# Optimization experiments

Hardware: AMD Instinct MI355X
Metric: run time of the kernel (lower is better)

## Reference

```python
import jax, jax.numpy as jnp
import numpy as np

B, T, D, H = 2, 2048, 1024, 16
HD = D // H
SCALE = HD ** -0.5
NEG_INF = float(np.finfo(np.float32).min)


def setup_inputs() -> dict:
    key = jax.random.key(0)
    ks = jax.random.split(key, 10)
    s = 1.0 / np.sqrt(D)
    x = jax.random.normal(ks[0], (B, T, D), dtype=jnp.float32)
    # causal mask, True = keep, shape (B,1,T,T)
    mask = jnp.broadcast_to(jnp.tril(jnp.ones((T, T), dtype=bool)), (B, 1, T, T))
    Wq = jax.random.normal(ks[1], (D, D), dtype=jnp.float32) * s
    bq = jax.random.normal(ks[2], (D,), dtype=jnp.float32) * s
    Wk = jax.random.normal(ks[3], (D, D), dtype=jnp.float32) * s
    bk = jax.random.normal(ks[4], (D,), dtype=jnp.float32) * s
    Wv = jax.random.normal(ks[5], (D, D), dtype=jnp.float32) * s
    bv = jax.random.normal(ks[6], (D,), dtype=jnp.float32) * s
    Wo = jax.random.normal(ks[7], (D, D), dtype=jnp.float32) * s
    bo = jax.random.normal(ks[8], (D,), dtype=jnp.float32) * s
    return {"x": x, "mask": mask, "Wq": Wq, "bq": bq, "Wk": Wk, "bk": bk,
            "Wv": Wv, "bv": bv, "Wo": Wo, "bo": bo}


def _split_heads(t):
    # (B,T,D) -> (B,H,T,HD)
    return t.reshape(B, T, H, HD).transpose(0, 2, 1, 3)


def masked_rowwise_softmax(scores, mask):
    # mask: bool, True = keep; fully-masked rows return zeros.
    s = scores.astype(jnp.float32)
    masked = jnp.where(mask, s, NEG_INF)
    row_max = jnp.max(masked, axis=-1, keepdims=True)
    exps = jnp.exp(masked - row_max) * mask.astype(jnp.float32)
    denom = jnp.maximum(jnp.sum(exps, axis=-1, keepdims=True), 1e-12)
    return (exps / denom).astype(scores.dtype)


def reference(x, mask, Wq, bq, Wk, bk, Wv, bv, Wo, bo):
    q = _split_heads(x @ Wq.T + bq)
    k = _split_heads(x @ Wk.T + bk)
    v = _split_heads(x @ Wv.T + bv)
    scores = jnp.einsum('bhqd,bhkd->bhqk', q, k) * SCALE
    m = jnp.broadcast_to(mask, (B, H, T, T))
    attn = masked_rowwise_softmax(scores, m)
    y = jnp.einsum('bhqk,bhkd->bhqd', attn, v)
    y = y.transpose(0, 2, 1, 3).reshape(B, T, D)
    return y @ Wo.T + bo
```

## Files before the change

### kernel.cpp

```cpp
#include <hip/hip_runtime.h>

#define B_ 2
#define H_ 16
#define T_ 2048
#define D_ 1024
#define HD_ 64
#define NEG_HUGE (-3.402823466e38f)
#define QSCALE 0.18033688011112042f

typedef unsigned short u16;
typedef unsigned int u32;
typedef __attribute__((ext_vector_type(8))) short bf16x8;
typedef __attribute__((ext_vector_type(4))) float f32x4;

__device__ __forceinline__ u16 f2bf(float f) {
    u32 u = __builtin_bit_cast(u32, f);
    u += 0x7FFFu + ((u >> 16) & 1u);
    return (u16)(u >> 16);
}

__device__ __forceinline__ u32 pk2bf(float f0, float f1) {
    const u32 a0 = __builtin_bit_cast(u32, f0) + 0x8000u;
    const u32 a1 = __builtin_bit_cast(u32, f1) + 0x8000u;
    return __builtin_amdgcn_perm(a1, a0, 0x07060302u);
}

__device__ __forceinline__ uint2 pk4bf(f32x4 a) {
    uint2 r;
    r.x = pk2bf(a[0], a[1]);
    r.y = pk2bf(a[2], a[3]);
    return r;
}

__device__ __forceinline__ f32x4 mfma16(bf16x8 a, bf16x8 b, f32x4 c) {
    return __builtin_amdgcn_mfma_f32_16x16x32_bf16(a, b, c, 0, 0, 0);
}

__device__ __forceinline__ void gld16(const void* g, void* l) {
    __builtin_amdgcn_global_load_lds(
        (const __attribute__((address_space(1))) u32*)g,
        (__attribute__((address_space(3))) u32*)l, 16, 0, 0);
}

__global__ __launch_bounds__(256) void to_bf16(
    const float* __restrict__ x,  const float* __restrict__ wq,
    const float* __restrict__ wk, const float* __restrict__ wv,
    const float* __restrict__ wo, u16* __restrict__ dst)
{
    const size_t g = ((size_t)blockIdx.x * 256 + threadIdx.x) * 8;
    const float* src; size_t off;
    if      (g < (size_t)(4u << 20)) { src = x;  off = g; }
    else if (g < (size_t)(5u << 20)) { src = wq; off = g - (size_t)(4u << 20); }
    else if (g < (size_t)(6u << 20)) { src = wk; off = g - (size_t)(5u << 20); }
    else if (g < (size_t)(7u << 20)) { src = wv; off = g - (size_t)(6u << 20); }
    else                             { src = wo; off = g - (size_t)(7u << 20); }
    const float4 a = *(const float4*)&src[off];
    const float4 b = *(const float4*)&src[off + 4];
    ushort4 lo = make_ushort4(f2bf(a.x), f2bf(a.y), f2bf(a.z), f2bf(a.w));
    ushort4 hi = make_ushort4(f2bf(b.x), f2bf(b.y), f2bf(b.z), f2bf(b.w));
    *(ushort4*)&dst[g]     = lo;
    *(ushort4*)&dst[g + 4] = hi;
}

__device__ __forceinline__ void gemm128_core(
    const u16* __restrict__ P0, const u16* __restrict__ P1,
    const int m0, const int n0, u16* As, u16* Bs, f32x4 (&acc)[4][4])
{
    const int tid  = threadIdx.x;
    const int lane = tid & 63;
    const int quad = lane >> 4;
    const int l15  = lane & 15;
    const int w    = tid >> 6;
    const int wm   = (w >> 1) << 6;
    const int wn   = (w & 1) << 6;
    const int swz  = l15 & 7;

    size_t aoff[4], boff[4];
    int    loff[4];
#pragma unroll
    for (int i = 0; i < 4; ++i) {
        const int slot = i * 256 + tid;
        const int r = slot >> 3, c = slot & 7;
        const int gc = ((c ^ (r & 7)) << 3);
        aoff[i] = (size_t)(m0 + r) * D_ + gc;
        boff[i] = (size_t)(n0 + r) * D_ + gc;
        loff[i] = slot * 8;
    }
    int rowA[4], rowB[4];
#pragma unroll
    for (int i = 0; i < 4; ++i) {
        rowA[i] = (wm + i * 16 + l15) * 64;
        rowB[i] = (wn + i * 16 + l15) * 64;
    }

    for (int k0 = 0; k0 < D_; k0 += 64) {
        __syncthreads();
#pragma unroll
        for (int i = 0; i < 4; ++i) {
            gld16(&P0[aoff[i] + k0], &As[loff[i]]);
            gld16(&P1[boff[i] + k0], &Bs[loff[i]]);
        }
        __syncthreads();
#pragma unroll
        for (int s = 0; s < 2; ++s) {
            const int ch = (((s << 2) + quad) ^ swz) << 3;
            bf16x8 af[4], bf[4];
#pragma unroll
            for (int mi = 0; mi < 4; ++mi) af[mi] = *(const bf16x8*)&As[rowA[mi] + ch];
#pragma unroll
            for (int ni = 0; ni < 4; ++ni) bf[ni] = *(const bf16x8*)&Bs[rowB[ni] + ch];
#pragma unroll
            for (int mi = 0; mi < 4; ++mi)
#pragma unroll
                for (int ni = 0; ni < 4; ++ni)
                    acc[mi][ni] = mfma16(af[mi], bf[ni], acc[mi][ni]);
        }
    }
}

__global__ __launch_bounds__(256) void gemm_qkv(
    const u16* __restrict__ xb,
    const u16* __restrict__ Wqb, const u16* __restrict__ Wkb, const u16* __restrict__ Wvb,
    const float* __restrict__ bq, const float* __restrict__ bk, const float* __restrict__ bv,
    u16* __restrict__ Qb, u16* __restrict__ Kb, u16* __restrict__ Vtb)
{
    __shared__ u16 As[128 * 64];
    __shared__ u16 Bs[128 * 64];
    const int z = blockIdx.z;

    f32x4 acc[4][4];
#pragma unroll
    for (int i = 0; i < 4; ++i)
#pragma unroll
        for (int j = 0; j < 4; ++j) acc[i][j] = (f32x4){0.f, 0.f, 0.f, 0.f};

    const int tid  = threadIdx.x;
    const int lane = tid & 63;
    const int quad = lane >> 4;
    const int l15  = lane & 15;
    const int w    = tid >> 6;
    const int wm   = (w >> 1) << 6;
    const int wn   = (w & 1) << 6;
    const int pq   = quad >> 1;
    const int psub = (quad & 1) << 2;

    u16* scr = ((w < 2) ? As : Bs) + ((w & 1) ? 4096 : 0);

    if (z < 2) {
        const u16*   W    = z ? Wkb : Wqb;
        const float* bias = z ? bk  : bq;
        const float  CF   = z ? 1.f : QSCALE;
        u16*         C    = z ? Kb  : Qb;
        const int m0 = blockIdx.x << 7;
        const int n0 = blockIdx.y << 7;
        gemm128_core(W, xb, m0, n0, As, Bs, acc);
        __syncthreads();

        const int fb = m0 + wm;
        const int h  = fb >> 6;
        const int tb = n0 + wn;
#pragma unroll
        for (int i = 0; i < 4; ++i) {
            const float4 bi = *(const float4*)&bias[fb + i * 16 + (quad << 2)];
#pragma unroll
            for (int j = 0; j < 4; ++j) {
                const int tl = j * 16 + l15;
                f32x4 a = acc[i][j];
                f32x4 v = { (a[0] + bi.x) * CF, (a[1] + bi.y) * CF,
                            (a[2] + bi.z) * CF, (a[3] + bi.w) * CF };
                *(uint2*)&scr[tl * 64 + (((2 * i + pq) ^ (tl & 7)) << 3) + psub] = pk4bf(v);
            }
        }
        __asm__ volatile("s_waitcnt lgkmcnt(0)" ::: "memory");

        const int b  = tb >> 11;
        const int t0 = tb & 2047;
#pragma unroll
        for (int e = 0; e < 8; ++e) {
            const int tl = (lane >> 3) + e * 8;
            const int c  = lane & 7;
            bf16x8 v = *(const bf16x8*)&scr[tl * 64 + ((c ^ (tl & 7)) << 3)];
            *(bf16x8*)&C[((size_t)((b << 4) + h) * T_ + t0 + tl) * HD_ + (c << 3)] = v;
        }
    } else {
        const int m0 = blockIdx.y << 7;
        const int n0 = blockIdx.x << 7;
        gemm128_core(xb, Wvb, m0, n0, As, Bs, acc);
        __syncthreads();

#pragma unroll
        for (int j = 0; j < 4; ++j) {
            const int row = j * 16 + l15;
            const float bi = bv[n0 + wn + row];
            const int sw = row & 7;
#pragma unroll
            for (int i = 0; i < 4; ++i) {
                f32x4 a = acc[i][j];
                f32x4 v = { a[0] + bi, a[1] + bi, a[2] + bi, a[3] + bi };
                *(uint2*)&scr[row * 64 + (((2 * i + pq) ^ sw) << 3) + psub] = pk4bf(v);
            }
        }
        __asm__ volatile("s_waitcnt lgkmcnt(0)" ::: "memory");

        const int b  = (m0 + wm) >> 11;
        const int t0 = (m0 + wm) & 2047;
        const int h  = (n0 + wn) >> 6;
#pragma unroll
        for (int e = 0; e < 8; ++e) {
            const int hdl = (lane >> 3) + e * 8;
            const int c   = lane & 7;
            bf16x8 vv = *(const bf16x8*)&scr[hdl * 64 + ((c ^ (hdl & 7)) << 3)];
            *(bf16x8*)&Vtb[((size_t)((b << 4) + h) * HD_ + hdl) * T_ + t0 + (c << 3)] = vv;
        }
    }
}

__global__ __launch_bounds__(256) void gemm_out(
    const u16* __restrict__ Ab, const u16* __restrict__ Wob,
    const float* __restrict__ bo, float* __restrict__ C)
{
    __shared__ u16 As[128 * 64];
    __shared__ u16 Bs[128 * 64];
    const int m0 = blockIdx.y << 7;
    const int n0 = blockIdx.x << 7;

    f32x4 acc[4][4];
#pragma unroll
    for (int i = 0; i < 4; ++i)
#pragma unroll
        for (int j = 0; j < 4; ++j) acc[i][j] = (f32x4){0.f, 0.f, 0.f, 0.f};

    gemm128_core(Ab, Wob, m0, n0, As, Bs, acc);

    const int tid  = threadIdx.x;
    const int lane = tid & 63;
    const int quad = lane >> 4;
    const int l15  = lane & 15;
    const int w    = tid >> 6;
    const int wm   = (w >> 1) << 6;
    const int wn   = (w & 1) << 6;

    float bi[4];
#pragma unroll
    for (int ni = 0; ni < 4; ++ni) bi[ni] = bo[n0 + wn + ni * 16 + l15];

#pragma unroll
    for (int mi = 0; mi < 4; ++mi) {
        const int m = m0 + wm + mi * 16 + (quad << 2);
#pragma unroll
        for (int r = 0; r < 4; ++r)
#pragma unroll
            for (int ni = 0; ni < 4; ++ni)
                C[(size_t)(m + r) * D_ + n0 + wn + ni * 16 + l15] = acc[mi][ni][r] + bi[ni];
    }
}

__global__ __launch_bounds__(256) void attn_mfma(
    const u16* __restrict__ Qg, const u16* __restrict__ Kg,
    const u16* __restrict__ Vtg, u16* __restrict__ Out)
{
    __shared__ u16 Ks[128 * 64];
    __shared__ u16 Vs[64 * 128];
    __shared__ u16 Ps[4 * 16 * 128];
    const int tid  = threadIdx.x;
    const int w    = tid >> 6;
    const int lane = tid & 63;
    const int quad = lane >> 4;
    const int l15  = lane & 15;
    const int bh   = blockIdx.x;
    const int yb   = blockIdx.y;
    const size_t base = (size_t)bh * (T_ * HD_);

    int lK[4], lV[4];
    size_t gK[4], gV[4];
#pragma unroll
    for (int i = 0; i < 4; ++i) {
        const int slot = i * 256 + tid;
        const int rk = slot >> 3, ck = slot & 7;
        lK[i] = rk * 64 + ((ck ^ (rk & 7)) << 3);
        gK[i] = base + (size_t)rk * HD_ + ck * 8;
        const int rv = slot >> 4, cv = slot & 15;
        lV[i] = rv * 128 + ((cv ^ (rv & 15)) << 3);
        gV[i] = base + (size_t)rv * T_ + cv * 8;
    }

    bf16x8 ones;
#pragma unroll
    for (int i = 0; i < 8; ++i) ones[i] = (short)0x3F80;

    u16* Pw = &Ps[w * 2048];
    const int swz7 = l15 & 7;
    const int pq   = quad >> 1;
    const int psub = (quad & 1) << 2;
    const int b = bh >> 4, h = bh & 15;

    for (int half = 0; half < 2; ++half) {
        const int qt = half ? yb : (31 - yb);
        const int qloc = (w << 4) + l15;
        const int qrow = (qt << 6) + qloc;
        const bf16x8 qf0 = *(const bf16x8*)&Qg[base + (size_t)qrow * HD_ + quad * 8];
        const bf16x8 qf1 = *(const bf16x8*)&Qg[base + (size_t)qrow * HD_ + 32 + quad * 8];

        f32x4 o[4];
#pragma unroll
        for (int nt = 0; nt < 4; ++nt) o[nt] = (f32x4){0.f, 0.f, 0.f, 0.f};
        f32x4 Lacc = (f32x4){0.f, 0.f, 0.f, 0.f};

        const int nIter = (qt + 2) >> 1;
        bf16x8 kreg[4], vreg[4];
#pragma unroll
        for (int i = 0; i < 4; ++i) {
            kreg[i] = *(const bf16x8*)&Kg[gK[i]];
            vreg[i] = *(const bf16x8*)&Vtg[gV[i]];
        }

        for (int it = 0; it < nIter; ++it) {
            __syncthreads();
#pragma unroll
            for (int i = 0; i < 4; ++i) {
                *(bf16x8*)&Ks[lK[i]] = kreg[i];
                *(bf16x8*)&Vs[lV[i]] = vreg[i];
            }
            if (it + 1 < nIter) {
                const int koff = (it + 1) << 7;
#pragma unroll
                for (int i = 0; i < 4; ++i) {
                    kreg[i] = *(const bf16x8*)&Kg[gK[i] + (size_t)koff * HD_];
                    vreg[i] = *(const bf16x8*)&Vtg[gV[i] + koff];
                }
            }
            __syncthreads();

            f32x4 st[8];
#pragma unroll
            for (int t = 0; t < 8; ++t) {
                const int kr = (t * 16 + l15) * 64;
                const bf16x8 k0 = *(const bf16x8*)&Ks[kr + ((quad ^ swz7) << 3)];
                const bf16x8 k1 = *(const bf16x8*)&Ks[kr + (((quad + 4) ^ swz7) << 3)];
                f32x4 a = (f32x4){0.f, 0.f, 0.f, 0.f};
                a = mfma16(k0, qf0, a);
                a = mfma16(k1, qf1, a);
                st[t] = a;
            }

            if (it == nIter - 1) {
                const int koff = it << 7;
#pragma unroll
                for (int t = 0; t < 8; ++t)
#pragma unroll
                    for (int r = 0; r < 4; ++r) {
                        const int kg = koff + t * 16 + (quad << 2) + r;
                        if (kg > qrow) st[t][r] = NEG_HUGE;
                    }
            }

#pragma unroll
            for (int t = 0; t < 8; ++t)
#pragma unroll
                for (int r = 0; r < 4; ++r) st[t][r] = exp2f(st[t][r]);

#pragma unroll
            for (int t = 0; t < 8; ++t)
                *(uint2*)&Pw[l15 * 128 + (((2 * t + pq) ^ l15) << 3) + psub] = pk4bf(st[t]);
            __asm__ volatile("s_waitcnt lgkmcnt(0)" ::: "memory");

            bf16x8 pf[4];
#pragma unroll
            for (int kq = 0; kq < 4; ++kq)
                pf[kq] = *(const bf16x8*)&Pw[l15 * 128 + ((((kq << 2) + quad) ^ l15) << 3)];

#pragma unroll
            for (int nt = 0; nt < 4; ++nt) {
                f32x4 oo = o[nt];
                const int vr = (nt * 16 + l15) * 128;
#pragma unroll
                for (int kq = 0; kq < 4; ++kq) {
                    const bf16x8 vf = *(const bf16x8*)&Vs[vr + ((((kq << 2) + quad) ^ l15) << 3)];
                    oo = mfma16(pf[kq], vf, oo);
                }
                o[nt] = oo;
            }
#pragma unroll
            for (int kq = 0; kq < 4; ++kq)
                Lacc = mfma16(pf[kq], ones, Lacc);
        }

        f32x4 linv;
#pragma unroll
        for (int r = 0; r < 4; ++r) linv[r] = 1.f / fmaxf(Lacc[r], 1e-30f);

#pragma unroll
        for (int nt = 0; nt < 4; ++nt)
#pragma unroll
            for (int r = 0; r < 4; ++r) {
                const int qg2 = (qt << 6) + (w << 4) + (quad << 2) + r;
                const u32 u = __builtin_bit_cast(u32, o[nt][r] * linv[r]) + 0x8000u;
                Out[(size_t)(b * T_ + qg2) * D_ + (h << 6) + nt * 16 + l15] = (u16)(u >> 16);
            }
    }
}

extern "C" void kernel_launch(void* const* d_in, const int* in_sizes, int n_in,
                              void* d_out, int out_size, void* d_ws, size_t ws_size,
                              hipStream_t stream)
{
    const float* x  = (const float*)d_in[0];
    const float* Wq = (const float*)d_in[2];
    const float* bq = (const float*)d_in[3];
    const float* Wk = (const float*)d_in[4];
    const float* bk = (const float*)d_in[5];
    const float* Wv = (const float*)d_in[6];
    const float* bv = (const float*)d_in[7];
    const float* Wo = (const float*)d_in[8];
    const float* bo = (const float*)d_in[9];
    float* out = (float*)d_out;

    const size_t M1 = (size_t)1 << 20;
    u16* wsu = (u16*)d_ws;
    u16* xb  = wsu;
    u16* wqb = wsu + 4 * M1;
    u16* wkb = wsu + 5 * M1;
    u16* wvb = wsu + 6 * M1;
    u16* wob = wsu + 7 * M1;
    u16* Qb  = wsu + 8 * M1;
    u16* Kb  = wsu + 12 * M1;
    u16* Vtb = wsu + 16 * M1;
    u16* AOb = wsu + 20 * M1;

    to_bf16<<<4096, 256, 0, stream>>>(x, Wq, Wk, Wv, Wo, wsu);

    dim3 gq(D_ / 128, (B_ * T_) / 128, 3);
    gemm_qkv<<<gq, 256, 0, stream>>>(xb, wqb, wkb, wvb, bq, bk, bv, Qb, Kb, Vtb);

    dim3 ga(B_ * H_, T_ / 128);
    attn_mfma<<<ga, 256, 0, stream>>>(Qb, Kb, Vtb, AOb);

    dim3 go(D_ / 128, (B_ * T_) / 128);
    gemm_out<<<go, 256, 0, stream>>>(AOb, wob, bo, out);
}
```

Measured before the change: 213.6 us.

## Fuse fp32-to-bf16 conversion into GEMM loads and remap blocks per XCD

Removes the standalone to_bf16 kernel. The GEMMs now read fp32 x and weights directly, convert them to bf16 in registers and store them to LDS. The global_load_lds direct copy is replaced by register-staged prefetching of the next K tile. Grids are flattened to 1D with an XCD-aware tile mapping to improve L2 locality. This saves one launch and a full write/read of the converted buffers, but doubles the global bytes read per tile and adds conversion ALU work and register pressure inside the GEMM loop.

```diff
diff --git a/kernel.cpp b/kernel.cpp
--- a/kernel.cpp
+++ b/kernel.cpp
@@ -13,12 +13,6 @@
 typedef __attribute__((ext_vector_type(8))) short bf16x8;
 typedef __attribute__((ext_vector_type(4))) float f32x4;
 
-__device__ __forceinline__ u16 f2bf(float f) {
-    u32 u = __builtin_bit_cast(u32, f);
-    u += 0x7FFFu + ((u >> 16) & 1u);
-    return (u16)(u >> 16);
-}
-
 __device__ __forceinline__ u32 pk2bf(float f0, float f1) {
     const u32 a0 = __builtin_bit_cast(u32, f0) + 0x8000u;
     const u32 a1 = __builtin_bit_cast(u32, f1) + 0x8000u;
@@ -36,34 +30,9 @@
     return __builtin_amdgcn_mfma_f32_16x16x32_bf16(a, b, c, 0, 0, 0);
 }
 
-__device__ __forceinline__ void gld16(const void* g, void* l) {
-    __builtin_amdgcn_global_load_lds(
-        (const __attribute__((address_space(1))) u32*)g,
-        (__attribute__((address_space(3))) u32*)l, 16, 0, 0);
-}
-
-__global__ __launch_bounds__(256) void to_bf16(
-    const float* __restrict__ x,  const float* __restrict__ wq,
-    const float* __restrict__ wk, const float* __restrict__ wv,
-    const float* __restrict__ wo, u16* __restrict__ dst)
-{
-    const size_t g = ((size_t)blockIdx.x * 256 + threadIdx.x) * 8;
-    const float* src; size_t off;
-    if      (g < (size_t)(4u << 20)) { src = x;  off = g; }
-    else if (g < (size_t)(5u << 20)) { src = wq; off = g - (size_t)(4u << 20); }
-    else if (g < (size_t)(6u << 20)) { src = wk; off = g - (size_t)(5u << 20); }
-    else if (g < (size_t)(7u << 20)) { src = wv; off = g - (size_t)(6u << 20); }
-    else                             { src = wo; off = g - (size_t)(7u << 20); }
-    const float4 a = *(const float4*)&src[off];
-    const float4 b = *(const float4*)&src[off + 4];
-    ushort4 lo = make_ushort4(f2bf(a.x), f2bf(a.y), f2bf(a.z), f2bf(a.w));
-    ushort4 hi = make_ushort4(f2bf(b.x), f2bf(b.y), f2bf(b.z), f2bf(b.w));
-    *(ushort4*)&dst[g]     = lo;
-    *(ushort4*)&dst[g + 4] = hi;
-}
-
+template<int A32, int B32>
 __device__ __forceinline__ void gemm128_core(
-    const u16* __restrict__ P0, const u16* __restrict__ P1,
+    const void* __restrict__ P0v, const void* __restrict__ P1v,
     const int m0, const int n0, u16* As, u16* Bs, f32x4 (&acc)[4][4])
 {
     const int tid  = threadIdx.x;
@@ -75,15 +44,13 @@
     const int wn   = (w & 1) << 6;
     const int swz  = l15 & 7;
 
-    size_t aoff[4], boff[4];
-    int    loff[4];
+    int loff[4], grow[4], gcol[4];
 #pragma unroll
     for (int i = 0; i < 4; ++i) {
         const int slot = i * 256 + tid;
         const int r = slot >> 3, c = slot & 7;
-        const int gc = ((c ^ (r & 7)) << 3);
-        aoff[i] = (size_t)(m0 + r) * D_ + gc;
-        boff[i] = (size_t)(n0 + r) * D_ + gc;
+        grow[i] = r;
+        gcol[i] = (c ^ (r & 7)) << 3;
         loff[i] = slot * 8;
     }
     int rowA[4], rowB[4];
@@ -93,40 +60,106 @@
         rowB[i] = (wn + i * 16 + l15) * 64;
     }
 
+    bf16x8 pa[4], pb[4];
+    float4 fa[4][2], fb[4][2];
+
+#pragma unroll
+    for (int i = 0; i < 4; ++i) {
+        if constexpr (A32) {
+            const float* A = (const float*)P0v;
+            const float* p = &A[(size_t)(m0 + grow[i]) * D_ + gcol[i]];
+            fa[i][0] = *(const float4*)p;
+            fa[i][1] = *(const float4*)(p + 4);
+        } else {
+            const u16* A = (const u16*)P0v;
+            pa[i] = *(const bf16x8*)&A[(size_t)(m0 + grow[i]) * D_ + gcol[i]];
+        }
+        if constexpr (B32) {
+            const float* Bp = (const float*)P1v;
+            const float* p = &Bp[(size_t)(n0 + grow[i]) * D_ + gcol[i]];
+            fb[i][0] = *(const float4*)p;
+            fb[i][1] = *(const float4*)(p + 4);
+        } else {
+            const u16* Bp = (const u16*)P1v;
+            pb[i] = *(const bf16x8*)&Bp[(size_t)(n0 + grow[i]) * D_ + gcol[i]];
+        }
+    }
+
     for (int k0 = 0; k0 < D_; k0 += 64) {
         __syncthreads();
 #pragma unroll
         for (int i = 0; i < 4; ++i) {
-            gld16(&P0[aoff[i] + k0], &As[loff[i]]);
-            gld16(&P1[boff[i] + k0], &Bs[loff[i]]);
+            if constexpr (A32) {
+                uint4 v = { pk2bf(fa[i][0].x, fa[i][0].y), pk2bf(fa[i][0].z, fa[i][0].w),
+                            pk2bf(fa[i][1].x, fa[i][1].y), pk2bf(fa[i][1].z, fa[i][1].w) };
+                *(uint4*)&As[loff[i]] = v;
+            } else {
+                *(bf16x8*)&As[loff[i]] = pa[i];
+            }
+            if constexpr (B32) {
+                uint4 v = { pk2bf(fb[i][0].x, fb[i][0].y), pk2bf(fb[i][0].z, fb[i][0].w),
+                            pk2bf(fb[i][1].x, fb[i][1].y), pk2bf(fb[i][1].z, fb[i][1].w) };
+                *(uint4*)&Bs[loff[i]] = v;
+            } else {
+                *(bf16x8*)&Bs[loff[i]] = pb[i];
+            }
+        }
+        if (k0 + 64 < D_) {
+            const int kn = k0 + 64;
+#pragma unroll
+            for (int i = 0; i < 4; ++i) {
+                if constexpr (A32) {
+                    const float* A = (const float*)P0v;
+                    const float* p = &A[(size_t)(m0 + grow[i]) * D_ + kn + gcol[i]];
+                    fa[i][0] = *(const float4*)p;
+                    fa[i][1] = *(const float4*)(p + 4);
+                } else {
+                    const u16* A = (const u16*)P0v;
+                    pa[i] = *(const bf16x8*)&A[(size_t)(m0 + grow[i]) * D_ + kn + gcol[i]];
+                }
+                if constexpr (B32) {
+                    const float* Bp = (const float*)P1v;
+                    const float* p = &Bp[(size_t)(n0 + grow[i]) * D_ + kn + gcol[i]];
+                    fb[i][0] = *(const float4*)p;
+                    fb[i][1] = *(const float4*)(p + 4);
+                } else {
+                    const u16* Bp = (const u16*)P1v;
+                    pb[i] = *(const bf16x8*)&Bp[(size_t)(n0 + grow[i]) * D_ + kn + gcol[i]];
+                }
+            }
         }
         __syncthreads();
 #pragma unroll
         for (int s = 0; s < 2; ++s) {
             const int ch = (((s << 2) + quad) ^ swz) << 3;
-            bf16x8 af[4], bf[4];
-#pragma unroll
-            for (int mi = 0; mi < 4; ++mi) af[mi] = *(const bf16x8*)&As[rowA[mi] + ch];
-#pragma unroll
-            for (int ni = 0; ni < 4; ++ni) bf[ni] = *(const bf16x8*)&Bs[rowB[ni] + ch];
+            bf16x8 am[4], bm[4];
+#pragma unroll
+            for (int mi = 0; mi < 4; ++mi) am[mi] = *(const bf16x8*)&As[rowA[mi] + ch];
+#pragma unroll
+            for (int ni = 0; ni < 4; ++ni) bm[ni] = *(const bf16x8*)&Bs[rowB[ni] + ch];
 #pragma unroll
             for (int mi = 0; mi < 4; ++mi)
 #pragma unroll
                 for (int ni = 0; ni < 4; ++ni)
-                    acc[mi][ni] = mfma16(af[mi], bf[ni], acc[mi][ni]);
+                    acc[mi][ni] = mfma16(am[mi], bm[ni], acc[mi][ni]);
         }
     }
 }
 
 __global__ __launch_bounds__(256) void gemm_qkv(
-    const u16* __restrict__ xb,
-    const u16* __restrict__ Wqb, const u16* __restrict__ Wkb, const u16* __restrict__ Wvb,
+    const float* __restrict__ x,
+    const float* __restrict__ Wq, const float* __restrict__ Wk, const float* __restrict__ Wv,
     const float* __restrict__ bq, const float* __restrict__ bk, const float* __restrict__ bv,
     u16* __restrict__ Qb, u16* __restrict__ Kb, u16* __restrict__ Vtb)
 {
     __shared__ u16 As[128 * 64];
     __shared__ u16 Bs[128 * 64];
-    const int z = blockIdx.z;
+    const int L   = blockIdx.x;
+    const int xcd = L & 7;
+    const int kk  = L >> 3;
+    const int tt  = (xcd << 2) + (kk & 3);
+    const int ft  = (kk >> 2) & 7;
+    const int z   = kk >> 5;
 
     f32x4 acc[4][4];
 #pragma unroll
@@ -147,13 +180,13 @@
     u16* scr = ((w < 2) ? As : Bs) + ((w & 1) ? 4096 : 0);
 
     if (z < 2) {
-        const u16*   W    = z ? Wkb : Wqb;
-        const float* bias = z ? bk  : bq;
+        const float* W    = z ? Wk : Wq;
+        const float* bias = z ? bk : bq;
         const float  CF   = z ? 1.f : QSCALE;
-        u16*         C    = z ? Kb  : Qb;
-        const int m0 = blockIdx.x << 7;
-        const int n0 = blockIdx.y << 7;
-        gemm128_core(W, xb, m0, n0, As, Bs, acc);
+        u16*         C    = z ? Kb : Qb;
+        const int m0 = ft << 7;
+        const int n0 = tt << 7;
+        gemm128_core<1, 1>(W, x, m0, n0, As, Bs, acc);
         __syncthreads();
 
         const int fb = m0 + wm;
@@ -183,9 +216,9 @@
             *(bf16x8*)&C[((size_t)((b << 4) + h) * T_ + t0 + tl) * HD_ + (c << 3)] = v;
         }
     } else {
-        const int m0 = blockIdx.y << 7;
-        const int n0 = blockIdx.x << 7;
-        gemm128_core(xb, Wvb, m0, n0, As, Bs, acc);
+        const int m0 = tt << 7;
+        const int n0 = ft << 7;
+        gemm128_core<1, 1>(x, Wv, m0, n0, As, Bs, acc);
         __syncthreads();
 
 #pragma unroll
@@ -216,13 +249,18 @@
 }
 
 __global__ __launch_bounds__(256) void gemm_out(
-    const u16* __restrict__ Ab, const u16* __restrict__ Wob,
+    const u16* __restrict__ Ab, const float* __restrict__ Wo,
     const float* __restrict__ bo, float* __restrict__ C)
 {
     __shared__ u16 As[128 * 64];
     __shared__ u16 Bs[128 * 64];
-    const int m0 = blockIdx.y << 7;
-    const int n0 = blockIdx.x << 7;
+    const int L   = blockIdx.x;
+    const int xcd = L & 7;
+    const int kk  = L >> 3;
+    const int tt  = (xcd << 2) + (kk & 3);
+    const int ft  = kk >> 2;
+    const int m0  = tt << 7;
+    const int n0  = ft << 7;
 
     f32x4 acc[4][4];
 #pragma unroll
@@ -230,7 +268,7 @@
 #pragma unroll
         for (int j = 0; j < 4; ++j) acc[i][j] = (f32x4){0.f, 0.f, 0.f, 0.f};
 
-    gemm128_core(Ab, Wob, m0, n0, As, Bs, acc);
+    gemm128_core<0, 1>(Ab, Wo, m0, n0, As, Bs, acc);
 
     const int tid  = threadIdx.x;
     const int lane = tid & 63;
@@ -417,24 +455,15 @@
 
     const size_t M1 = (size_t)1 << 20;
     u16* wsu = (u16*)d_ws;
-    u16* xb  = wsu;
-    u16* wqb = wsu + 4 * M1;
-    u16* wkb = wsu + 5 * M1;
-    u16* wvb = wsu + 6 * M1;
-    u16* wob = wsu + 7 * M1;
-    u16* Qb  = wsu + 8 * M1;
-    u16* Kb  = wsu + 12 * M1;
-    u16* Vtb = wsu + 16 * M1;
-    u16* AOb = wsu + 20 * M1;
-
-    to_bf16<<<4096, 256, 0, stream>>>(x, Wq, Wk, Wv, Wo, wsu);
-
-    dim3 gq(D_ / 128, (B_ * T_) / 128, 3);
-    gemm_qkv<<<gq, 256, 0, stream>>>(xb, wqb, wkb, wvb, bq, bk, bv, Qb, Kb, Vtb);
+    u16* Qb  = wsu;
+    u16* Kb  = wsu + 4 * M1;
+    u16* Vtb = wsu + 8 * M1;
+    u16* AOb = wsu + 12 * M1;
+
+    gemm_qkv<<<768, 256, 0, stream>>>(x, Wq, Wk, Wv, bq, bk, bv, Qb, Kb, Vtb);
 
     dim3 ga(B_ * H_, T_ / 128);
     attn_mfma<<<ga, 256, 0, stream>>>(Qb, Kb, Vtb, AOb);
 
-    dim3 go(D_ / 128, (B_ * T_) / 128);
-    gemm_out<<<go, 256, 0, stream>>>(AOb, wob, bo, out);
-}
+    gemm_out<<<256, 256, 0, stream>>>(AOb, Wo, bo, out);
+}
```

Result: no change. 212.7 us (-0.4%).

## Register-prefetch GEMM tiles and remap GEMM blocks for XCD-aware locality

Applied to the files above, without the earlier changes.

Replaces direct global-to-LDS loads in the shared GEMM core with register prefetch. The next K-slice is loaded into registers while the current slice is computed, then stored to LDS. It also flattens the QKV and output GEMM grids into 1D launches with a remapping that groups token tiles by XCD (blockIdx & 7), to improve L2 reuse of the activation rows. This raises register pressure and adds an extra VGPR-to-LDS store per tile, while aiming to overlap global latency with MFMA work.

```diff
diff --git a/kernel.cpp b/kernel.cpp
--- a/kernel.cpp
+++ b/kernel.cpp
@@ -34,12 +34,6 @@
 
 __device__ __forceinline__ f32x4 mfma16(bf16x8 a, bf16x8 b, f32x4 c) {
     return __builtin_amdgcn_mfma_f32_16x16x32_bf16(a, b, c, 0, 0, 0);
-}
-
-__device__ __forceinline__ void gld16(const void* g, void* l) {
-    __builtin_amdgcn_global_load_lds(
-        (const __attribute__((address_space(1))) u32*)g,
-        (__attribute__((address_space(3))) u32*)l, 16, 0, 0);
 }
 
 __global__ __launch_bounds__(256) void to_bf16(
@@ -81,7 +75,7 @@
     for (int i = 0; i < 4; ++i) {
         const int slot = i * 256 + tid;
         const int r = slot >> 3, c = slot & 7;
-        const int gc = ((c ^ (r & 7)) << 3);
+        const int gc = (c ^ (r & 7)) << 3;
         aoff[i] = (size_t)(m0 + r) * D_ + gc;
         boff[i] = (size_t)(n0 + r) * D_ + gc;
         loff[i] = slot * 8;
@@ -93,27 +87,42 @@
         rowB[i] = (wn + i * 16 + l15) * 64;
     }
 
+    bf16x8 pa[4], pb[4];
+#pragma unroll
+    for (int i = 0; i < 4; ++i) {
+        pa[i] = *(const bf16x8*)&P0[aoff[i]];
+        pb[i] = *(const bf16x8*)&P1[boff[i]];
+    }
+
     for (int k0 = 0; k0 < D_; k0 += 64) {
         __syncthreads();
 #pragma unroll
         for (int i = 0; i < 4; ++i) {
-            gld16(&P0[aoff[i] + k0], &As[loff[i]]);
-            gld16(&P1[boff[i] + k0], &Bs[loff[i]]);
+            *(bf16x8*)&As[loff[i]] = pa[i];
+            *(bf16x8*)&Bs[loff[i]] = pb[i];
+        }
+        if (k0 + 64 < D_) {
+            const int kn = k0 + 64;
+#pragma unroll
+            for (int i = 0; i < 4; ++i) {
+                pa[i] = *(const bf16x8*)&P0[aoff[i] + kn];
+                pb[i] = *(const bf16x8*)&P1[boff[i] + kn];
+            }
         }
         __syncthreads();
 #pragma unroll
         for (int s = 0; s < 2; ++s) {
             const int ch = (((s << 2) + quad) ^ swz) << 3;
-            bf16x8 af[4], bf[4];
-#pragma unroll
-            for (int mi = 0; mi < 4; ++mi) af[mi] = *(const bf16x8*)&As[rowA[mi] + ch];
-#pragma unroll
-            for (int ni = 0; ni < 4; ++ni) bf[ni] = *(const bf16x8*)&Bs[rowB[ni] + ch];
+            bf16x8 am[4], bm[4];
+#pragma unroll
+            for (int mi = 0; mi < 4; ++mi) am[mi] = *(const bf16x8*)&As[rowA[mi] + ch];
+#pragma unroll
+            for (int ni = 0; ni < 4; ++ni) bm[ni] = *(const bf16x8*)&Bs[rowB[ni] + ch];
 #pragma unroll
             for (int mi = 0; mi < 4; ++mi)
 #pragma unroll
                 for (int ni = 0; ni < 4; ++ni)
-                    acc[mi][ni] = mfma16(af[mi], bf[ni], acc[mi][ni]);
+                    acc[mi][ni] = mfma16(am[mi], bm[ni], acc[mi][ni]);
         }
     }
 }
@@ -126,7 +135,12 @@
 {
     __shared__ u16 As[128 * 64];
     __shared__ u16 Bs[128 * 64];
-    const int z = blockIdx.z;
+    const int L   = blockIdx.x;
+    const int xcd = L & 7;
+    const int kk  = L >> 3;
+    const int tt  = (xcd << 2) + (kk & 3);
+    const int ft  = (kk >> 2) & 7;
+    const int z   = kk >> 5;
 
     f32x4 acc[4][4];
 #pragma unroll
@@ -151,8 +165,8 @@
         const float* bias = z ? bk  : bq;
         const float  CF   = z ? 1.f : QSCALE;
         u16*         C    = z ? Kb  : Qb;
-        const int m0 = blockIdx.x << 7;
-        const int n0 = blockIdx.y << 7;
+        const int m0 = ft << 7;
+        const int n0 = tt << 7;
         gemm128_core(W, xb, m0, n0, As, Bs, acc);
         __syncthreads();
 
@@ -183,8 +197,8 @@
             *(bf16x8*)&C[((size_t)((b << 4) + h) * T_ + t0 + tl) * HD_ + (c << 3)] = v;
         }
     } else {
-        const int m0 = blockIdx.y << 7;
-        const int n0 = blockIdx.x << 7;
+        const int m0 = tt << 7;
+        const int n0 = ft << 7;
         gemm128_core(xb, Wvb, m0, n0, As, Bs, acc);
         __syncthreads();
 
@@ -221,8 +235,13 @@
 {
     __shared__ u16 As[128 * 64];
     __shared__ u16 Bs[128 * 64];
-    const int m0 = blockIdx.y << 7;
-    const int n0 = blockIdx.x << 7;
+    const int L   = blockIdx.x;
+    const int xcd = L & 7;
+    const int kk  = L >> 3;
+    const int tt  = (xcd << 2) + (kk & 3);
+    const int ft  = kk >> 2;
+    const int m0  = tt << 7;
+    const int n0  = ft << 7;
 
     f32x4 acc[4][4];
 #pragma unroll
@@ -429,12 +448,10 @@
 
     to_bf16<<<4096, 256, 0, stream>>>(x, Wq, Wk, Wv, Wo, wsu);
 
-    dim3 gq(D_ / 128, (B_ * T_) / 128, 3);
-    gemm_qkv<<<gq, 256, 0, stream>>>(xb, wqb, wkb, wvb, bq, bk, bv, Qb, Kb, Vtb);
+    gemm_qkv<<<768, 256, 0, stream>>>(xb, wqb, wkb, wvb, bq, bk, bv, Qb, Kb, Vtb);
 
     dim3 ga(B_ * H_, T_ / 128);
     attn_mfma<<<ga, 256, 0, stream>>>(Qb, Kb, Vtb, AOb);
 
-    dim3 go(D_ / 128, (B_ * T_) / 128);
-    gemm_out<<<go, 256, 0, stream>>>(AOb, wob, bo, out);
-}
+    gemm_out<<<256, 256, 0, stream>>>(AOb, wob, bo, out);
+}
```

New measurement: 195.5 us. 8.5% less time.
